# Kernel tuning notes

Hardware: AMD Instinct MI355X
Metric: run time of the kernel (lower is better)

Reference implementation:

```python
import jax, jax.numpy as jnp
import numpy as np

U, N, L, C, D, B = 50000, 50000, 10, 256, 64, 4096


def setup_inputs() -> dict:
    key = jax.random.key(0)
    ks = jax.random.split(key, 12)
    xav = float(np.sqrt(6.0 / (D + D)))  # xavier_uniform bound for [D, D]
    return {
        "items": jax.random.randint(ks[0], (U, L), 0, N),
        "time_embs": jax.random.normal(ks[1], (U, L, D), dtype=jnp.float32),
        "user_embedding": jax.random.normal(ks[2], (U, D), dtype=jnp.float32),
        "item_embedding": jax.random.normal(ks[3], (N, D), dtype=jnp.float32),
        "cluster_emb": jax.random.normal(ks[4], (C, D), dtype=jnp.float32),
        "w_filters": jax.random.normal(ks[5], (U, L, D), dtype=jnp.float32),
        "Wq": jax.random.uniform(ks[6], (D, D), jnp.float32, -xav, xav),
        "Wk": jax.random.uniform(ks[7], (D, D), jnp.float32, -xav, xav),
        "Wv": jax.random.uniform(ks[8], (D, D), jnp.float32, -xav, xav),
        "users": jax.random.randint(ks[9], (B,), 0, U),
        "pos_items": jax.random.randint(ks[10], (B,), 0, N),
        "neg_items": jax.random.randint(ks[11], (B,), 0, N),
        "alpha1": jnp.float32(1.0),
        "alpha2": jnp.float32(1.0),
        "alpha3": jnp.float32(1.0),
    }


def reference(items, time_embs, user_embedding, item_embedding, cluster_emb,
              w_filters, Wq, Wk, Wv, users, pos_items, neg_items,
              alpha1, alpha2, alpha3):
    d = Wq.shape[0]
    # short_items_embs built under torch.no_grad / .detach() in the original
    short = jax.lax.stop_gradient(
        user_embedding[:, None, :] + item_embedding[items] + time_embs)  # [U,L,D]
    Q = short @ Wq                                   # [U,L,D]
    K = cluster_emb @ Wk                             # [C,D]
    V = cluster_emb @ Wv                             # [C,D]
    scores = jnp.einsum("uld,cd->ulc", Q, K) / jnp.sqrt(jnp.float32(d))
    attn = jax.nn.softmax(scores, axis=-1)           # [U,L,C]
    shorted = jnp.einsum("ulc,cd->uld", attn, V)     # [U,L,D]
    # matrix_filter = shorted^T @ w_filter per user -> [U,D,D]
    mfilt = jnp.einsum("uld,ule->ude", shorted, w_filters)
    new_user = jnp.einsum("ud,ude->ue", user_embedding, mfilt)  # [U,D]
    mix = alpha3 * (alpha1 * user_embedding + alpha2 * new_user)
    u_g = mix[users]                     # [B,D]
    pos_g = item_embedding[pos_items]    # [B,D]
    neg_g = item_embedding[neg_items]    # [B,D]
    return (u_g, pos_g, neg_g)
```

## Files before the change

kernel.cpp:

```cpp
#include <hip/hip_runtime.h>

#define D 64
#define L 10
#define C 256
#define G 8
#define SWB 72

typedef __attribute__((ext_vector_type(8))) short bf16x8;
typedef __attribute__((ext_vector_type(4))) short short4v;
typedef __attribute__((ext_vector_type(4))) float f32x4;

__device__ inline short f2bf(float f) {
  unsigned u = __float_as_uint(f);
  u = (u + 0x7FFFu + ((u >> 16) & 1u)) >> 16;
  return (short)u;
}
__device__ inline float4 add3(float4 a, float4 b, float4 c) {
  return make_float4(a.x + b.x + c.x, a.y + b.y + c.y, a.z + b.z + c.z, a.w + b.w + c.w);
}
__device__ inline short4v f2bf4(float4 a) {
  short4v r;
  r[0] = f2bf(a.x); r[1] = f2bf(a.y); r[2] = f2bf(a.z); r[3] = f2bf(a.w);
  return r;
}

__global__ __launch_bounds__(256) void pre(const float* __restrict__ cl,
                                           const float* __restrict__ Wk,
                                           const float* __restrict__ Wq,
                                           const float* __restrict__ Wv,
                                           short* __restrict__ Bf) {
  __shared__ float s_cl[4 * 64];
  __shared__ float s_kc[4 * 64];
  __shared__ float s_w[64 * 65];
  const int t = threadIdx.x;
  const int bh = blockIdx.x >> 6, cb = blockIdx.x & 63;
  const int c0 = cb * 4;
  const int r = t >> 6, j = t & 63;

  s_cl[t] = cl[c0 * 64 + t];
  if (bh == 0) {
#pragma unroll
    for (int i = 0; i < 4; ++i) {
      int e = i * 256 + t;
      float4 v = ((const float4*)Wq)[e];
      int k = e >> 4, q = e & 15;
      float* dst = &s_w[k * 65 + q * 4];
      dst[0] = v.x; dst[1] = v.y; dst[2] = v.z; dst[3] = v.w;
    }
  }
  __syncthreads();

  const float* __restrict__ Wx = bh ? Wv : Wk;
  float acc = 0.f;
#pragma unroll 8
  for (int m = 0; m < 64; ++m) acc += s_cl[r * 64 + m] * Wx[m * 64 + j];

  if (bh == 1) {
    Bf[(c0 + r) * 128 + 64 + j] = f2bf(acc);
    return;
  }
  s_kc[t] = acc;
  __syncthreads();

  float o = 0.f;
#pragma unroll 8
  for (int jj = 0; jj < 64; ++jj) o += s_kc[r * 64 + jj] * s_w[j * 65 + jj];
  Bf[(c0 + r) * 128 + j] = f2bf(0.125f * o);
}

__global__ __launch_bounds__(256) void filter_main(
    const int* __restrict__ items, const float* __restrict__ te,
    const float* __restrict__ ue_g, const float* __restrict__ ie_g,
    const float* __restrict__ wf_g, const short* __restrict__ Bf,
    const int* __restrict__ users, const int* __restrict__ pos_items,
    const int* __restrict__ neg_items, const float* __restrict__ a1p,
    const float* __restrict__ a2p, const float* __restrict__ a3p,
    float* __restrict__ out, int B) {
  __shared__ short s_shb[88 * SWB];
  __shared__ float2 s_red[G][12][4];

  const int tid = threadIdx.x, w = tid >> 6, lane = tid & 63;
  const int col16 = lane & 15, kb = lane >> 4;
  const int qr = col16 >> 2, jr = col16 & 3;
  const int b8 = blockIdx.x * G;
  const int BD = B * D;

  const int uA = users[b8 + w], uB = users[b8 + 4 + w];
  const float uevA = ue_g[uA * D + lane];
  const float uevB = ue_g[uB * D + lane];
  const float posvA = ie_g[pos_items[b8 + w] * D + lane];
  const float posvB = ie_g[pos_items[b8 + 4 + w] * D + lane];
  const float negvA = ie_g[neg_items[b8 + w] * D + lane];
  const float negvB = ie_g[neg_items[b8 + 4 + w] * D + lane];
  float wfvA[L], wfvB[L];
#pragma unroll
  for (int l = 0; l < L; ++l) {
    wfvA[l] = wf_g[(uA * L + l) * D + lane];
    wfvB[l] = wf_g[(uB * L + l) * D + lane];
  }

  {
    const float4* te4 = (const float4*)te;
    const float4* ie4 = (const float4*)ie_g;
    const float4* ue4 = (const float4*)ue_g;
    const int grp = tid >> 4, j = tid & 15;
#pragma unroll
    for (int it = 0; it < 6; ++it) {
      int row = it * 16 + grp;
      if (row < 80) {
        int g = row / 10, l = row - g * 10;
        int u = users[b8 + g];
        int itm = items[u * L + l];
        float4 v = add3(te4[(u * L + l) * 16 + j], ie4[itm * 16 + j],
                        ue4[u * 16 + j]);
        *(short4v*)&s_shb[row * SWB + j * 4] = f2bf4(v);
      } else if (row < 88) {
        int u = users[b8 + (row - 80)];
        *(short4v*)&s_shb[row * SWB + j * 4] = f2bf4(ue4[u * 16 + j]);
      }
    }
  }
  __syncthreads();

  bf16x8 af[6][2];
  bf16x8 au0 = {}, au1 = {};
#pragma unroll
  for (int mt = 0; mt < 6; ++mt) {
    int p = mt * 4 + jr;
    int g = p / 3;
    int l = (p - g * 3) * 4 + qr;
    if (l < L) {
      const bf16x8* rp = (const bf16x8*)&s_shb[(g * 10 + l) * SWB];
      af[mt][0] = rp[kb];
      af[mt][1] = rp[4 + kb];
    } else {
      af[mt][0] = bf16x8{};
      af[mt][1] = bf16x8{};
    }
  }
  if (col16 < G) {
    const bf16x8* rp = (const bf16x8*)&s_shb[(80 + col16) * SWB];
    au0 = rp[kb];
    au1 = rp[4 + kb];
  }

  float Sa[6][4], Ta[6][4];
#pragma unroll
  for (int mt = 0; mt < 6; ++mt)
#pragma unroll
    for (int jj = 0; jj < 4; ++jj) { Sa[mt][jj] = 0.f; Ta[mt][jj] = 0.f; }

#pragma unroll
  for (int nt = 0; nt < 4; ++nt) {
    const bf16x8* bp = (const bf16x8*)(Bf + ((w * 4 + nt) * 16 + col16) * 128);
    bf16x8 b0 = bp[kb], b1 = bp[4 + kb], b2 = bp[8 + kb], b3 = bp[12 + kb];
    f32x4 z = {0.f, 0.f, 0.f, 0.f};
    f32x4 cc[6];
    f32x4 cu = z;
#pragma unroll
    for (int mt = 0; mt < 6; ++mt) {
      cc[mt] = z;
      cc[mt] = __builtin_amdgcn_mfma_f32_16x16x32_bf16(af[mt][0], b0, cc[mt], 0, 0, 0);
      cc[mt] = __builtin_amdgcn_mfma_f32_16x16x32_bf16(af[mt][1], b1, cc[mt], 0, 0, 0);
    }
    cu = __builtin_amdgcn_mfma_f32_16x16x32_bf16(au0, b2, cu, 0, 0, 0);
    cu = __builtin_amdgcn_mfma_f32_16x16x32_bf16(au1, b3, cu, 0, 0, 0);
    float vub[8];
#pragma unroll
    for (int g = 0; g < 8; ++g)
      vub[g] = __shfl(cu[g & 3], (g >> 2) * 16 + col16, 64);
#pragma unroll
    for (int mt = 0; mt < 6; ++mt)
#pragma unroll
      for (int jj = 0; jj < 4; ++jj) {
        float e = __expf(cc[mt][jj]);
        const int g = (mt * 4 + jj) / 3;
        Sa[mt][jj] += e;
        Ta[mt][jj] += e * vub[g];
      }
  }

#pragma unroll
  for (int mt = 0; mt < 6; ++mt)
#pragma unroll
    for (int jj = 0; jj < 4; ++jj) {
      float S = Sa[mt][jj], T = Ta[mt][jj];
      S += __shfl_xor(S, 1, 64); T += __shfl_xor(T, 1, 64);
      S += __shfl_xor(S, 2, 64); T += __shfl_xor(T, 2, 64);
      S += __shfl_xor(S, 4, 64); T += __shfl_xor(T, 4, 64);
      S += __shfl_xor(S, 8, 64); T += __shfl_xor(T, 8, 64);
      if (col16 == 0) {
        const int g = (mt * 4 + jj) / 3, sub = (mt * 4 + jj) % 3;
        s_red[g][sub * 4 + kb][w] = make_float2(S, T);
      }
    }
  __syncthreads();

  float nuA = 0.f, nuB = 0.f;
#pragma unroll
  for (int l = 0; l < L; ++l) {
    {
      float2 p0 = s_red[w][l][0], p1 = s_red[w][l][1];
      float2 p2 = s_red[w][l][2], p3 = s_red[w][l][3];
      float S = (p0.x + p1.x) + (p2.x + p3.x);
      float T = (p0.y + p1.y) + (p2.y + p3.y);
      nuA += T * __frcp_rn(S) * wfvA[l];
    }
    {
      float2 p0 = s_red[w + 4][l][0], p1 = s_red[w + 4][l][1];
      float2 p2 = s_red[w + 4][l][2], p3 = s_red[w + 4][l][3];
      float S = (p0.x + p1.x) + (p2.x + p3.x);
      float T = (p0.y + p1.y) + (p2.y + p3.y);
      nuB += T * __frcp_rn(S) * wfvB[l];
    }
  }
  const float a1 = *a1p, a2 = *a2p, a3 = *a3p;
  out[(b8 + w) * D + lane] = a3 * (a1 * uevA + a2 * nuA);
  out[(b8 + 4 + w) * D + lane] = a3 * (a1 * uevB + a2 * nuB);
  out[BD + (b8 + w) * D + lane] = posvA;
  out[BD + (b8 + 4 + w) * D + lane] = posvB;
  out[2 * BD + (b8 + w) * D + lane] = negvA;
  out[2 * BD + (b8 + 4 + w) * D + lane] = negvB;
}

extern "C" void kernel_launch(void* const* d_in, const int* in_sizes, int n_in,
                              void* d_out, int out_size, void* d_ws, size_t ws_size,
                              hipStream_t stream) {
  const int* items = (const int*)d_in[0];
  const float* time_embs = (const float*)d_in[1];
  const float* user_emb = (const float*)d_in[2];
  const float* item_emb = (const float*)d_in[3];
  const float* cluster = (const float*)d_in[4];
  const float* wf = (const float*)d_in[5];
  const float* Wq = (const float*)d_in[6];
  const float* Wk = (const float*)d_in[7];
  const float* Wv = (const float*)d_in[8];
  const int* users = (const int*)d_in[9];
  const int* pos = (const int*)d_in[10];
  const int* neg = (const int*)d_in[11];
  const float* a1 = (const float*)d_in[12];
  const float* a2 = (const float*)d_in[13];
  const float* a3 = (const float*)d_in[14];
  const int B = in_sizes[9];

  short* Bf = (short*)d_ws;
  hipLaunchKernelGGL(pre, dim3(128), dim3(256), 0, stream,
                     cluster, Wk, Wq, Wv, Bf);
  hipLaunchKernelGGL(filter_main, dim3(B / G), dim3(256), 0, stream,
                     items, time_embs, user_emb, item_emb, wf, Bf,
                     users, pos, neg, a1, a2, a3, (float*)d_out, B);
}
```

Measured before the change: 28.76 us.

## Fuse precompute into main kernel with a global atomic flag barrier

Merges the K/V projection precompute kernel into the main filter kernel. The first 128 blocks compute the projected cluster matrix, then signal completion through an agent-scope atomic counter. Every block spins on that counter before its MFMA phase, so the gathers overlap with the precompute and one kernel launch boundary goes away. In exchange it adds a memset launch, spin-wait traffic, and a larger shared-memory footprint per block. Correctness depends on the 128 producer blocks being scheduled, which is likely with 512 blocks but not guaranteed.

```diff
diff --git a/kernel.cpp b/kernel.cpp
--- a/kernel.cpp
+++ b/kernel.cpp
@@ -5,6 +5,7 @@
 #define C 256
 #define G 8
 #define SWB 72
+#define NPRE 128
 
 typedef __attribute__((ext_vector_type(8))) short bf16x8;
 typedef __attribute__((ext_vector_type(4))) short short4v;
@@ -24,65 +25,27 @@
   return r;
 }
 
-__global__ __launch_bounds__(256) void pre(const float* __restrict__ cl,
-                                           const float* __restrict__ Wk,
-                                           const float* __restrict__ Wq,
-                                           const float* __restrict__ Wv,
-                                           short* __restrict__ Bf) {
+__global__ __launch_bounds__(256) void fused(
+    const int* __restrict__ items, const float* __restrict__ te,
+    const float* __restrict__ ue_g, const float* __restrict__ ie_g,
+    const float* __restrict__ wf_g, const float* __restrict__ cl,
+    const float* __restrict__ Wq, const float* __restrict__ Wk,
+    const float* __restrict__ Wv, const int* __restrict__ users,
+    const int* __restrict__ pos_items, const int* __restrict__ neg_items,
+    const float* __restrict__ a1p, const float* __restrict__ a2p,
+    const float* __restrict__ a3p, int* __restrict__ flag,
+    short* __restrict__ Bf, float* __restrict__ out, int B) {
+  __shared__ float s_w[64 * 65];
   __shared__ float s_cl[4 * 64];
   __shared__ float s_kc[4 * 64];
-  __shared__ float s_w[64 * 65];
-  const int t = threadIdx.x;
-  const int bh = blockIdx.x >> 6, cb = blockIdx.x & 63;
-  const int c0 = cb * 4;
-  const int r = t >> 6, j = t & 63;
-
-  s_cl[t] = cl[c0 * 64 + t];
-  if (bh == 0) {
-#pragma unroll
-    for (int i = 0; i < 4; ++i) {
-      int e = i * 256 + t;
-      float4 v = ((const float4*)Wq)[e];
-      int k = e >> 4, q = e & 15;
-      float* dst = &s_w[k * 65 + q * 4];
-      dst[0] = v.x; dst[1] = v.y; dst[2] = v.z; dst[3] = v.w;
-    }
-  }
-  __syncthreads();
-
-  const float* __restrict__ Wx = bh ? Wv : Wk;
-  float acc = 0.f;
-#pragma unroll 8
-  for (int m = 0; m < 64; ++m) acc += s_cl[r * 64 + m] * Wx[m * 64 + j];
-
-  if (bh == 1) {
-    Bf[(c0 + r) * 128 + 64 + j] = f2bf(acc);
-    return;
-  }
-  s_kc[t] = acc;
-  __syncthreads();
-
-  float o = 0.f;
-#pragma unroll 8
-  for (int jj = 0; jj < 64; ++jj) o += s_kc[r * 64 + jj] * s_w[j * 65 + jj];
-  Bf[(c0 + r) * 128 + j] = f2bf(0.125f * o);
-}
-
-__global__ __launch_bounds__(256) void filter_main(
-    const int* __restrict__ items, const float* __restrict__ te,
-    const float* __restrict__ ue_g, const float* __restrict__ ie_g,
-    const float* __restrict__ wf_g, const short* __restrict__ Bf,
-    const int* __restrict__ users, const int* __restrict__ pos_items,
-    const int* __restrict__ neg_items, const float* __restrict__ a1p,
-    const float* __restrict__ a2p, const float* __restrict__ a3p,
-    float* __restrict__ out, int B) {
   __shared__ short s_shb[88 * SWB];
   __shared__ float2 s_red[G][12][4];
 
+  const int bid = blockIdx.x;
   const int tid = threadIdx.x, w = tid >> 6, lane = tid & 63;
   const int col16 = lane & 15, kb = lane >> 4;
   const int qr = col16 >> 2, jr = col16 & 3;
-  const int b8 = blockIdx.x * G;
+  const int b8 = bid * G;
   const int BD = B * D;
 
   const int uA = users[b8 + w], uB = users[b8 + 4 + w];
@@ -97,6 +60,41 @@
   for (int l = 0; l < L; ++l) {
     wfvA[l] = wf_g[(uA * L + l) * D + lane];
     wfvB[l] = wf_g[(uB * L + l) * D + lane];
+  }
+
+  if (bid < NPRE) {
+    const int bh = bid >> 6, cb = bid & 63;
+    const int c0 = cb * 4;
+    const int r = tid >> 6, j = tid & 63;
+    s_cl[tid] = cl[c0 * 64 + tid];
+    if (bh == 0) {
+#pragma unroll
+      for (int i = 0; i < 4; ++i) {
+        int e = i * 256 + tid;
+        float4 v = ((const float4*)Wq)[e];
+        int k = e >> 4, q = e & 15;
+        float* dst = &s_w[k * 65 + q * 4];
+        dst[0] = v.x; dst[1] = v.y; dst[2] = v.z; dst[3] = v.w;
+      }
+    }
+    __syncthreads();
+    const float* __restrict__ Wx = bh ? Wv : Wk;
+    float acc = 0.f;
+#pragma unroll 8
+    for (int m = 0; m < 64; ++m) acc += s_cl[r * 64 + m] * Wx[m * 64 + j];
+    if (bh == 1) {
+      Bf[(c0 + r) * 128 + 64 + j] = f2bf(acc);
+    } else {
+      s_kc[tid] = acc;
+      __syncthreads();
+      float o = 0.f;
+#pragma unroll 8
+      for (int jj = 0; jj < 64; ++jj) o += s_kc[r * 64 + jj] * s_w[j * 65 + jj];
+      Bf[(c0 + r) * 128 + j] = f2bf(0.125f * o);
+    }
+    __syncthreads();
+    if (tid == 0)
+      __hip_atomic_fetch_add(flag, 1, __ATOMIC_RELEASE, __HIP_MEMORY_SCOPE_AGENT);
   }
 
   {
@@ -143,6 +141,13 @@
     au0 = rp[kb];
     au1 = rp[4 + kb];
   }
+
+  if (tid == 0) {
+    while (__hip_atomic_load(flag, __ATOMIC_ACQUIRE, __HIP_MEMORY_SCOPE_AGENT) <
+           NPRE)
+      __builtin_amdgcn_s_sleep(8);
+  }
+  __syncthreads();
 
   float Sa[6][4], Ta[6][4];
 #pragma unroll
@@ -243,10 +248,11 @@
   const float* a3 = (const float*)d_in[14];
   const int B = in_sizes[9];
 
-  short* Bf = (short*)d_ws;
-  hipLaunchKernelGGL(pre, dim3(128), dim3(256), 0, stream,
-                     cluster, Wk, Wq, Wv, Bf);
-  hipLaunchKernelGGL(filter_main, dim3(B / G), dim3(256), 0, stream,
-                     items, time_embs, user_emb, item_emb, wf, Bf,
-                     users, pos, neg, a1, a2, a3, (float*)d_out, B);
-}
+  int* flag = (int*)d_ws;
+  short* Bf = (short*)d_ws + 32;
+  hipMemsetAsync(flag, 0, 4, stream);
+  hipLaunchKernelGGL(fused, dim3(B / G), dim3(256), 0, stream,
+                     items, time_embs, user_emb, item_emb, wf, cluster,
+                     Wq, Wk, Wv, users, pos, neg, a1, a2, a3,
+                     flag, Bf, (float*)d_out, B);
+}
```

Result: slower. 38.90 us (+35.3%).
